# Performance work log

Hardware: AMD Instinct MI355X
Metric: run time of the kernel (lower is better)

The kernel has to match this reference:

```python
import jax, jax.numpy as jnp
import numpy as np

DIM = 64
NUM_HEAD = 4
C_IN = 2 * DIM                      # dim * proj_ratio
N_PER_HEAD = C_IN // NUM_HEAD       # 32
M_TRI = N_PER_HEAD * (N_PER_HEAD + 1) // 2   # 528
C_POOL = NUM_HEAD * M_TRI           # 2112 == dim*(dim+2)/2
EPS = 1e-5


def setup_inputs() -> dict:
    key = jax.random.key(0)
    ks = jax.random.split(key, 8)
    B, H, W = 4, 128, 128
    x = jax.random.normal(ks[0], (B, C_IN, H, W), dtype=jnp.float32)
    norm1_w = 1.0 + 0.1 * jax.random.normal(ks[1], (C_IN,), dtype=jnp.float32)
    norm1_b = 0.1 * jax.random.normal(ks[2], (C_IN,), dtype=jnp.float32)
    dr_w = 0.02 * jax.random.normal(ks[3], (DIM, C_POOL), dtype=jnp.float32)
    dr_b = 0.02 * jax.random.normal(ks[4], (DIM,), dtype=jnp.float32)
    norm2_w = 1.0 + 0.1 * jax.random.normal(ks[5], (DIM,), dtype=jnp.float32)
    norm2_b = 0.1 * jax.random.normal(ks[6], (DIM,), dtype=jnp.float32)
    fc1_w = 0.05 * jax.random.normal(ks[7], (DIM, DIM), dtype=jnp.float32)
    fc1_b = jnp.zeros((DIM,), dtype=jnp.float32)
    return {"x": x, "norm1_w": norm1_w, "norm1_b": norm1_b,
            "dr_w": dr_w, "dr_b": dr_b,
            "norm2_w": norm2_w, "norm2_b": norm2_b,
            "fc1_w": fc1_w, "fc1_b": fc1_b}


def _layernorm_nchw(x, g, b):
    # LayerNorm over channel dim of NCHW tensor (torch permutes to NHWC first)
    xt = jnp.transpose(x, (0, 2, 3, 1))
    mu = jnp.mean(xt, axis=-1, keepdims=True)
    var = jnp.mean(jnp.square(xt - mu), axis=-1, keepdims=True)
    y = (xt - mu) / jnp.sqrt(var + EPS) * g + b
    return jnp.transpose(y, (0, 3, 1, 2))


def reference(x, norm1_w, norm1_b, dr_w, dr_b, norm2_w, norm2_b, fc1_w, fc1_b):
    B, C, H, W = x.shape
    L = H * W
    nh, n = NUM_HEAD, N_PER_HEAD

    # --- norm1 ---
    x = _layernorm_nchw(x, norm1_w, norm1_b)

    # --- MHSP ---
    # channel shuffle: group = C // num_head = n, group_C = num_head
    x = x.reshape(B, n, nh, H, W).transpose(0, 2, 1, 3, 4).reshape(B, C, H, W)
    # unfold with kernel=1, stride=1, pad=0 is a pure reshape -> [B, L, C]
    t = x.reshape(B, C, L).transpose(0, 2, 1).reshape(B, L, nh, n)
    # per-position per-head rank-1 outer product: [B, L, nh, n, n]
    outer = jnp.einsum('blhi,blhj->blhij', t, t)
    # sparse_mapping matmul == gather of upper-triangle entries (row-major i<=j)
    iu, ju = np.triu_indices(n)
    pf = outer[..., iu, ju]                      # [B, L, nh, m]
    pf = pf.reshape(B, L, nh * M_TRI).transpose(0, 2, 1).reshape(B, C_POOL, H, W)

    # --- CTM token mixer ---
    C2 = C_POOL
    y = pf.reshape(B, nh, C2 // nh, L)
    yn = y / jnp.linalg.norm(y, axis=2, keepdims=True)
    mid = L // 2
    x0 = yn[..., mid]                            # [B, nh, C2/nh]
    attn = jnp.einsum('bhc,bhcl->bhl', x0, yn)   # [B, nh, L]
    attn = jax.nn.softmax(attn, axis=-1)[:, :, None, :]
    y = (y * attn * float(L)).reshape(B, C2, H, W)

    # --- dimension reduction (1x1 conv) ---
    z = jnp.einsum('bchw,oc->bohw', y, dr_w) + dr_b[None, :, None, None]

    # --- norm2 + LightMlp (1x1 conv + GELU) ---
    z = _layernorm_nchw(z, norm2_w, norm2_b)
    z = jnp.einsum('bchw,oc->bohw', z, fc1_w) + fc1_b[None, :, None, None]
    z = jax.nn.gelu(z, approximate=False)
    return z
```

## Files before the change

kernel.cpp:

```cpp
#include <hip/hip_runtime.h>
#include <hip/hip_bf16.h>
#include <math.h>

#define B_    4
#define CIN   128
#define L_    16384
#define NH    4
#define NN    32
#define MT    528
#define CP    2112
#define DIM_  64
#define LT    64
#define MID   8192
#define EPS_  1e-5f

#define KPH   640
#define KTOT  2560
#define WSWN  (KTOT * DIM_)
#define FSWN  (2 * 4 * 64 * 8)
#define LOGITS_BLOCKS 1024
#define PREP_BLOCKS   656

typedef __attribute__((ext_vector_type(8))) short short8;
typedef __attribute__((ext_vector_type(4))) float float4v;

__device__ inline unsigned short f2bf(float f) {
  unsigned u = __float_as_uint(f);
  unsigned r = (u + 0x7fffu + ((u >> 16) & 1u)) >> 16;
  return (unsigned short)r;
}
__device__ inline float bf2f(unsigned short h) {
  return __uint_as_float(((unsigned)h) << 16);
}

__device__ inline void kb_decode(int id, int& i, int& jb) {
  if (id < 32)      { i = id >> 2;               jb = id & 3; }
  else if (id < 56) { int r = id - 32; int d = r / 3; i = 8 + d;  jb = 1 + (r - 3 * d); }
  else if (id < 72) { int r = id - 56; i = 16 + (r >> 1); jb = 2 + (r & 1); }
  else              { i = 24 + (id - 72);         jb = 3; }
}

__global__ __launch_bounds__(256) void k_pre(const float* __restrict__ dr_w,
                                             const float* __restrict__ fc1_w,
                                             const float* __restrict__ x,
                                             const float* __restrict__ g1,
                                             const float* __restrict__ b1,
                                             unsigned short* __restrict__ wsw,
                                             unsigned short* __restrict__ fsw,
                                             float* __restrict__ ws_a,
                                             float* __restrict__ ws_bsum) {
  if (blockIdx.x >= LOGITS_BLOCKS) {
    int s = (blockIdx.x - LOGITS_BLOCKS) * 256 + threadIdx.x;
    if (s < WSWN) {
      int j    = s & 7;
      int lane = (s >> 3) & 63;
      int ot   = (s >> 9) & 3;
      int ksg  = s >> 11;
      int o  = ot * 16 + (lane & 15);
      int kp = ksg * 32 + (lane >> 4) * 8 + j;
      int h  = kp / KPH;
      int kk = kp - h * KPH;
      int kb = kk >> 3, jo = kk & 7;
      int i, jb; kb_decode(kb, i, jb);
      int jch = jb * 8 + jo;
      float val = 0.f;
      if (jch >= i) {
        int fi = 32 * i - (i * (i - 1)) / 2;
        int m  = h * MT + fi + (jch - i);
        val = dr_w[(size_t)o * CP + m];
      }
      wsw[s] = f2bf(val);
    } else {
      int s2 = s - WSWN;
      int j    = s2 & 7;
      int lane = (s2 >> 3) & 63;
      int ot   = (s2 >> 9) & 3;
      int ks2  = s2 >> 11;
      int o = ot * 16 + (lane & 15);
      int c = ks2 * 32 + (lane >> 4) * 8 + j;
      fsw[s2] = f2bf(fc1_w[o * DIM_ + c]);
    }
    return;
  }
  int blk = blockIdx.x;
  int b = blk >> 8;
  int l0 = (blk & 255) << 6;
  int t = threadIdx.x;
  int l = t & 63, q = t >> 6;
  __shared__ float xs[CIN], smid[CIN];
  __shared__ float part[4][64], part2[4][64], mu_s[64], isd_s[64];
  __shared__ float musd[2];

  if (t < CIN) xs[t] = x[(size_t)b * CIN * L_ + (size_t)t * L_ + MID];

  float tv[32];
  const float* xb = x + (size_t)b * CIN * L_ + l0 + l;
  float s = 0.f, s2 = 0.f;
#pragma unroll
  for (int cc = 0; cc < 32; cc++) {
    float v = xb[(size_t)(cc * 4 + q) * L_];
    tv[cc] = v; s += v; s2 += v * v;
  }
  part[q][l] = s; part2[q][l] = s2;
  __syncthreads();
  if (t == 0) {
    float su = 0.f;
    for (int c = 0; c < CIN; c++) su += xs[c];
    float mu = su / CIN;
    float sv = 0.f;
    for (int c = 0; c < CIN; c++) { float d = xs[c] - mu; sv += d * d; }
    musd[0] = mu; musd[1] = rsqrtf(sv / CIN + EPS_);
  }
  if (t < 64) {
    float su = part[0][t] + part[1][t] + part[2][t] + part[3][t];
    float su2 = part2[0][t] + part2[1][t] + part2[2][t] + part2[3][t];
    float mu = su * (1.f / CIN);
    float var = su2 * (1.f / CIN) - mu * mu;
    mu_s[t] = mu; isd_s[t] = rsqrtf(var + EPS_);
  }
  __syncthreads();
  if (t < CIN) {
    int c = ((t & 31) << 2) + (t >> 5);
    smid[t] = (xs[c] - musd[0]) * musd[1] * g1[c] + b1[c];
  }
  {
    float mu = mu_s[l], isd = isd_s[l];
#pragma unroll
    for (int cc = 0; cc < 32; cc++) {
      int co = cc * 4 + q;
      tv[cc] = (tv[cc] - mu) * isd * g1[co] + b1[co];
    }
  }
  __syncthreads();
  float T2 = 0.f, T4 = 0.f, st = 0.f, sc2 = 0.f, S2 = 0.f, S4 = 0.f;
#pragma unroll
  for (int i = 0; i < 32; i++) {
    float si = smid[q * 32 + i];
    float ti = tv[i];
    float t2 = ti * ti;
    T2 += t2; T4 = fmaf(t2, t2, T4);
    float ci = si * ti;
    st += ci; sc2 = fmaf(ci, ci, sc2);
    float s2i = si * si;
    S2 += s2i; S4 = fmaf(s2i, s2i, S4);
  }
  float num = 0.5f * (st * st + sc2);
  float logit = num * rsqrtf(0.25f * (T2 * T2 + T4) * (S2 * S2 + S4));
  float e = expf(logit - 1.f);
  ws_a[((size_t)b * NH + q) * L_ + l0 + l] = e;
  float ws = e;
#pragma unroll
  for (int mk = 1; mk < 64; mk <<= 1) ws += __shfl_xor(ws, mk, 64);
  if (l == 0) ws_bsum[((size_t)b * NH + q) * 256 + (blk & 255)] = ws;
}

struct __align__(16) SmemM {
  union __align__(16) { unsigned short p2[4 * 5 * 4 * 16 * 8]; float zb[64 * 65]; } u1;
  union __align__(16) { unsigned short ut[64 * 128]; unsigned short zn2[4 * 2 * 4 * 16 * 8]; } u2;
  float part[4][64], part2[4][64], mu_s[64], isd_s[64];
};

__device__ inline int utidx(int l, int c) {
  return l * 128 + ((((c >> 3) ^ (l & 7))) << 3) + (c & 7);
}

__global__ __launch_bounds__(256, 3) void k_main(const float* __restrict__ x,
      const float* __restrict__ g1, const float* __restrict__ b1,
      const float* __restrict__ dr_b,
      const float* __restrict__ g2, const float* __restrict__ b2,
      const float* __restrict__ fc1_b,
      const unsigned short* __restrict__ wsw, const unsigned short* __restrict__ fsw,
      const float* __restrict__ ws_a, const float* __restrict__ ws_bsum,
      float* __restrict__ out) {
  __shared__ SmemM sm;
  int blk = blockIdx.x;
  int b = blk >> 8;
  int l0 = (blk & 255) << 6;
  int t = threadIdx.x;
  int l = t & 63, q = t >> 6;

  float asum;
  {
    const float* bs = ws_bsum + ((size_t)b * NH + q) * 256;
    float a0 = bs[l] + bs[l + 64] + bs[l + 128] + bs[l + 192];
#pragma unroll
    for (int mk = 1; mk < 64; mk <<= 1) a0 += __shfl_xor(a0, mk, 64);
    asum = a0;
  }
  float e = ws_a[((size_t)b * NH + q) * L_ + l0 + l];
  float sa = sqrtf(e * ((float)L_ / asum));

  const float* xb = x + (size_t)b * CIN * L_ + l0;
  float s = 0.f, s2 = 0.f;
#pragma unroll
  for (int cb = 0; cb < 4; cb++) {
    unsigned short pk[8];
#pragma unroll
    for (int e8 = 0; e8 < 8; e8++) {
      int cc = cb * 8 + e8;
      int co = cc * 4 + q;
      float v = xb[(size_t)co * L_ + l];
      s += v; s2 += v * v;
      pk[e8] = f2bf(v);
    }
    *(short8*)&sm.u2.ut[l * 128 + (((q * 4 + cb) ^ (l & 7)) << 3)] = *(short8*)pk;
  }
  sm.part[q][l] = s; sm.part2[q][l] = s2;
  __syncthreads();
  if (t < 64) {
    float su = sm.part[0][t] + sm.part[1][t] + sm.part[2][t] + sm.part[3][t];
    float su2 = sm.part2[0][t] + sm.part2[1][t] + sm.part2[2][t] + sm.part2[3][t];
    float mu = su * (1.f / CIN);
    float var = su2 * (1.f / CIN) - mu * mu;
    sm.mu_s[t] = mu; sm.isd_s[t] = rsqrtf(var + EPS_);
  }
  __syncthreads();
  {
    float mu = sm.mu_s[l], isd = sm.isd_s[l];
#pragma unroll
    for (int cb = 0; cb < 4; cb++) {
      unsigned short* pp = &sm.u2.ut[l * 128 + (((q * 4 + cb) ^ (l & 7)) << 3)];
      short8 v8 = *(short8*)pp;
      unsigned short pk[8];
#pragma unroll
      for (int e8 = 0; e8 < 8; e8++) {
        int cc = cb * 8 + e8;
        int co = cc * 4 + q;
        float tvv = (bf2f((unsigned short)v8[e8]) - mu) * isd * g1[co] + b1[co];
        pk[e8] = f2bf(tvv * sa);
      }
      *(short8*)pp = *(short8*)pk;
    }
  }
  __syncthreads();

  const int otp = q & 1, ltp = q >> 1;
  const int lta = ltp * 2, ltb = ltp * 2 + 1;
  float4v acc[2][2];
  acc[0][0] = (float4v)0.f; acc[0][1] = (float4v)0.f;
  acc[1][0] = (float4v)0.f; acc[1][1] = (float4v)0.f;
  int tl = l;
  int ltile = l >> 4, n = l & 15;

  for (int cc16 = 0; cc16 < 16; cc16++) {
    int h = cc16 >> 2;
    int cpart = cc16 & 3;
#pragma unroll
    for (int s5 = 0; s5 < 5; s5++) {
      int kbl = q * 5 + s5;
      int kbh = cpart * 20 + kbl;
      int i, jb; kb_decode(kbh, i, jb);
      float ui = bf2f(sm.u2.ut[utidx(l, h * 32 + i)]);
      short8 ub = *(short8*)&sm.u2.ut[l * 128 + (((h * 4 + jb) ^ (l & 7)) << 3)];
      unsigned short pk[8];
#pragma unroll
      for (int e8 = 0; e8 < 8; e8++) pk[e8] = f2bf(ui * bf2f((unsigned short)ub[e8]));
      int ks = kbl >> 2, quad = kbl & 3;
      *(short8*)&sm.u1.p2[(((ltile * 5 + ks) * 4 + quad) * 16 + n) * 8] = *(short8*)pk;
    }
    __syncthreads();
#pragma unroll
    for (int ks = 0; ks < 5; ks++) {
      const unsigned short* wk = wsw + (size_t)(cc16 * 5 + ks) * 2048 + otp * 1024 + tl * 8;
      short8 a0 = *(const short8*)(wk);
      short8 a1 = *(const short8*)(wk + 512);
      short8 b0 = *(short8*)&sm.u1.p2[((lta * 5 + ks) * 64 + tl) * 8];
      short8 b1v = *(short8*)&sm.u1.p2[((ltb * 5 + ks) * 64 + tl) * 8];
      acc[0][0] = __builtin_amdgcn_mfma_f32_16x16x32_bf16(a0, b0,  acc[0][0], 0, 0, 0);
      acc[0][1] = __builtin_amdgcn_mfma_f32_16x16x32_bf16(a0, b1v, acc[0][1], 0, 0, 0);
      acc[1][0] = __builtin_amdgcn_mfma_f32_16x16x32_bf16(a1, b0,  acc[1][0], 0, 0, 0);
      acc[1][1] = __builtin_amdgcn_mfma_f32_16x16x32_bf16(a1, b1v, acc[1][1], 0, 0, 0);
    }
    __syncthreads();
  }

  int quad = tl >> 4;
#pragma unroll
  for (int oi = 0; oi < 2; oi++) {
#pragma unroll
    for (int li = 0; li < 2; li++) {
      int ot = otp * 2 + oi, ltx = ltp * 2 + li;
#pragma unroll
      for (int r = 0; r < 4; r++) {
        int o = ot * 16 + quad * 4 + r;
        sm.u1.zb[(ltx * 16 + n) * 65 + o] = acc[oi][li][r] + dr_b[o];
      }
    }
  }
  __syncthreads();
  {
    float ss = 0.f, ss2 = 0.f;
#pragma unroll
    for (int k = 0; k < 16; k++) {
      float v = sm.u1.zb[l * 65 + q * 16 + k];
      ss += v; ss2 += v * v;
    }
    sm.part[q][l] = ss; sm.part2[q][l] = ss2;
  }
  __syncthreads();
  if (t < 64) {
    float su = sm.part[0][t] + sm.part[1][t] + sm.part[2][t] + sm.part[3][t];
    float su2 = sm.part2[0][t] + sm.part2[1][t] + sm.part2[2][t] + sm.part2[3][t];
    float mu = su * (1.f / DIM_);
    float var = su2 * (1.f / DIM_) - mu * mu;
    sm.mu_s[t] = mu; sm.isd_s[t] = rsqrtf(var + EPS_);
  }
  __syncthreads();
  {
    float mu2 = sm.mu_s[l], isd2 = sm.isd_s[l];
#pragma unroll
    for (int kk = 0; kk < 2; kk++) {
      int kb2 = q * 2 + kk;
      int c0 = kb2 * 8;
      unsigned short pk[8];
#pragma unroll
      for (int e8 = 0; e8 < 8; e8++) {
        int c = c0 + e8;
        float v = (sm.u1.zb[l * 65 + c] - mu2) * isd2 * g2[c] + b2[c];
        pk[e8] = f2bf(v);
      }
      int ks2 = kb2 >> 2, qd2 = kb2 & 3;
      *(short8*)&sm.u2.zn2[(((ltile * 2 + ks2) * 4 + qd2) * 16 + n) * 8] = *(short8*)pk;
    }
  }
  __syncthreads();
  float4v acc2[4];
  acc2[0] = (float4v)0.f; acc2[1] = (float4v)0.f; acc2[2] = (float4v)0.f; acc2[3] = (float4v)0.f;
#pragma unroll
  for (int ks2 = 0; ks2 < 2; ks2++) {
    short8 bz = *(short8*)&sm.u2.zn2[((q * 2 + ks2) * 64 + tl) * 8];
    const unsigned short* fk = fsw + ks2 * 2048 + tl * 8;
    short8 f0 = *(const short8*)(fk);
    short8 f1 = *(const short8*)(fk + 512);
    short8 f2 = *(const short8*)(fk + 1024);
    short8 f3 = *(const short8*)(fk + 1536);
    acc2[0] = __builtin_amdgcn_mfma_f32_16x16x32_bf16(f0, bz, acc2[0], 0, 0, 0);
    acc2[1] = __builtin_amdgcn_mfma_f32_16x16x32_bf16(f1, bz, acc2[1], 0, 0, 0);
    acc2[2] = __builtin_amdgcn_mfma_f32_16x16x32_bf16(f2, bz, acc2[2], 0, 0, 0);
    acc2[3] = __builtin_amdgcn_mfma_f32_16x16x32_bf16(f3, bz, acc2[3], 0, 0, 0);
  }
#pragma unroll
  for (int ot = 0; ot < 4; ot++) {
#pragma unroll
    for (int r = 0; r < 4; r++) {
      int o2 = ot * 16 + quad * 4 + r;
      float sv = acc2[ot][r] + fc1_b[o2];
      float g = 0.5f * sv * (1.f + erff(sv * 0.70710678118f));
      out[((size_t)b * DIM_ + o2) * L_ + l0 + q * 16 + n] = g;
    }
  }
}

extern "C" void kernel_launch(void* const* d_in, const int* in_sizes, int n_in,
                              void* d_out, int out_size, void* d_ws, size_t ws_size,
                              hipStream_t stream) {
  const float* x    = (const float*)d_in[0];
  const float* n1w  = (const float*)d_in[1];
  const float* n1b  = (const float*)d_in[2];
  const float* drw  = (const float*)d_in[3];
  const float* drb  = (const float*)d_in[4];
  const float* n2w  = (const float*)d_in[5];
  const float* n2b  = (const float*)d_in[6];
  const float* fc1w = (const float*)d_in[7];
  const float* fc1b = (const float*)d_in[8];
  float* out = (float*)d_out;
  float* ws = (float*)d_ws;
  float* ws_a    = ws;
  float* ws_bsum = ws_a + (size_t)B_ * NH * L_;
  unsigned short* wsw = (unsigned short*)(ws_bsum + B_ * NH * 256);
  unsigned short* fsw = wsw + WSWN;

  hipLaunchKernelGGL(k_pre, dim3(LOGITS_BLOCKS + PREP_BLOCKS), dim3(256), 0, stream,
                     drw, fc1w, x, n1w, n1b, wsw, fsw, ws_a, ws_bsum);
  hipLaunchKernelGGL(k_main, dim3(B_ * (L_ / LT)), dim3(256), 0, stream,
                     x, n1w, n1b, drb, n2w, n2b, fc1b, wsw, fsw, ws_a, ws_bsum, out);
}
```

Before: 152.2 us.

## Repartition MFMA tiles per wave, pack bf16 pairs with perm, widen LDS swizzle

Each wave now computes all 64 output channels for its own 16-position tile, loading four weight fragments and one LDS B fragment per k-step instead of two of each. This cuts LDS reads of the product tile but doubles global weight loads per wave. Float-to-bf16 conversion now packs two values at once with a single perm on rounded-up bits (round-half-up rather than round-to-nearest-even). The LDS swizzle XOR widens from 8 to 16 lanes, and launch bounds rise to 4 blocks per SIMD, which may raise register pressure or cause spills.

```diff
diff --git a/kernel.cpp b/kernel.cpp
--- a/kernel.cpp
+++ b/kernel.cpp
@@ -31,6 +31,10 @@
 }
 __device__ inline float bf2f(unsigned short h) {
   return __uint_as_float(((unsigned)h) << 16);
+}
+__device__ inline unsigned pack2bf(float a, float b) {
+  return __builtin_amdgcn_perm(__float_as_uint(b) + 0x8000u,
+                               __float_as_uint(a) + 0x8000u, 0x07060302u);
 }
 
 __device__ inline void kb_decode(int id, int& i, int& jb) {
@@ -161,10 +165,10 @@
 };
 
 __device__ inline int utidx(int l, int c) {
-  return l * 128 + ((((c >> 3) ^ (l & 7))) << 3) + (c & 7);
-}
-
-__global__ __launch_bounds__(256, 3) void k_main(const float* __restrict__ x,
+  return l * 128 + ((((c >> 3) ^ (l & 15))) << 3) + (c & 7);
+}
+
+__global__ __launch_bounds__(256, 4) void k_main(const float* __restrict__ x,
       const float* __restrict__ g1, const float* __restrict__ b1,
       const float* __restrict__ dr_b,
       const float* __restrict__ g2, const float* __restrict__ b2,
@@ -194,16 +198,16 @@
   float s = 0.f, s2 = 0.f;
 #pragma unroll
   for (int cb = 0; cb < 4; cb++) {
-    unsigned short pk[8];
-#pragma unroll
-    for (int e8 = 0; e8 < 8; e8++) {
-      int cc = cb * 8 + e8;
-      int co = cc * 4 + q;
-      float v = xb[(size_t)co * L_ + l];
-      s += v; s2 += v * v;
-      pk[e8] = f2bf(v);
-    }
-    *(short8*)&sm.u2.ut[l * 128 + (((q * 4 + cb) ^ (l & 7)) << 3)] = *(short8*)pk;
+    unsigned pk[4];
+#pragma unroll
+    for (int e2 = 0; e2 < 4; e2++) {
+      int cc0 = cb * 8 + 2 * e2;
+      float v0 = xb[(size_t)(cc0 * 4 + q) * L_ + l];
+      float v1 = xb[(size_t)((cc0 + 1) * 4 + q) * L_ + l];
+      s += v0 + v1; s2 += v0 * v0 + v1 * v1;
+      pk[e2] = pack2bf(v0, v1);
+    }
+    *(short8*)&sm.u2.ut[l * 128 + (((q * 4 + cb) ^ (l & 15)) << 3)] = *(short8*)pk;
   }
   sm.part[q][l] = s; sm.part2[q][l] = s2;
   __syncthreads();
@@ -219,26 +223,24 @@
     float mu = sm.mu_s[l], isd = sm.isd_s[l];
 #pragma unroll
     for (int cb = 0; cb < 4; cb++) {
-      unsigned short* pp = &sm.u2.ut[l * 128 + (((q * 4 + cb) ^ (l & 7)) << 3)];
+      unsigned short* pp = &sm.u2.ut[l * 128 + (((q * 4 + cb) ^ (l & 15)) << 3)];
       short8 v8 = *(short8*)pp;
-      unsigned short pk[8];
-#pragma unroll
-      for (int e8 = 0; e8 < 8; e8++) {
-        int cc = cb * 8 + e8;
-        int co = cc * 4 + q;
-        float tvv = (bf2f((unsigned short)v8[e8]) - mu) * isd * g1[co] + b1[co];
-        pk[e8] = f2bf(tvv * sa);
+      unsigned pk[4];
+#pragma unroll
+      for (int e2 = 0; e2 < 4; e2++) {
+        int cc0 = cb * 8 + 2 * e2;
+        int co0 = cc0 * 4 + q, co1 = (cc0 + 1) * 4 + q;
+        float t0 = ((bf2f((unsigned short)v8[2 * e2])     - mu) * isd * g1[co0] + b1[co0]) * sa;
+        float t1 = ((bf2f((unsigned short)v8[2 * e2 + 1]) - mu) * isd * g1[co1] + b1[co1]) * sa;
+        pk[e2] = pack2bf(t0, t1);
       }
       *(short8*)pp = *(short8*)pk;
     }
   }
   __syncthreads();
 
-  const int otp = q & 1, ltp = q >> 1;
-  const int lta = ltp * 2, ltb = ltp * 2 + 1;
-  float4v acc[2][2];
-  acc[0][0] = (float4v)0.f; acc[0][1] = (float4v)0.f;
-  acc[1][0] = (float4v)0.f; acc[1][1] = (float4v)0.f;
+  float4v acc[4];
+  acc[0] = (float4v)0.f; acc[1] = (float4v)0.f; acc[2] = (float4v)0.f; acc[3] = (float4v)0.f;
   int tl = l;
   int ltile = l >> 4, n = l & 15;
 
@@ -251,40 +253,42 @@
       int kbh = cpart * 20 + kbl;
       int i, jb; kb_decode(kbh, i, jb);
       float ui = bf2f(sm.u2.ut[utidx(l, h * 32 + i)]);
-      short8 ub = *(short8*)&sm.u2.ut[l * 128 + (((h * 4 + jb) ^ (l & 7)) << 3)];
-      unsigned short pk[8];
-#pragma unroll
-      for (int e8 = 0; e8 < 8; e8++) pk[e8] = f2bf(ui * bf2f((unsigned short)ub[e8]));
+      short8 ub = *(short8*)&sm.u2.ut[l * 128 + (((h * 4 + jb) ^ (l & 15)) << 3)];
+      unsigned pk[4];
+#pragma unroll
+      for (int e2 = 0; e2 < 4; e2++) {
+        float p0 = ui * bf2f((unsigned short)ub[2 * e2]);
+        float p1 = ui * bf2f((unsigned short)ub[2 * e2 + 1]);
+        pk[e2] = pack2bf(p0, p1);
+      }
       int ks = kbl >> 2, quad = kbl & 3;
       *(short8*)&sm.u1.p2[(((ltile * 5 + ks) * 4 + quad) * 16 + n) * 8] = *(short8*)pk;
     }
     __syncthreads();
+    const unsigned short* wbase = wsw + (size_t)(cc16 * 5) * 2048 + tl * 8;
 #pragma unroll
     for (int ks = 0; ks < 5; ks++) {
-      const unsigned short* wk = wsw + (size_t)(cc16 * 5 + ks) * 2048 + otp * 1024 + tl * 8;
+      short8 bf = *(short8*)&sm.u1.p2[((q * 5 + ks) * 64 + tl) * 8];
+      const unsigned short* wk = wbase + ks * 2048;
       short8 a0 = *(const short8*)(wk);
       short8 a1 = *(const short8*)(wk + 512);
-      short8 b0 = *(short8*)&sm.u1.p2[((lta * 5 + ks) * 64 + tl) * 8];
-      short8 b1v = *(short8*)&sm.u1.p2[((ltb * 5 + ks) * 64 + tl) * 8];
-      acc[0][0] = __builtin_amdgcn_mfma_f32_16x16x32_bf16(a0, b0,  acc[0][0], 0, 0, 0);
-      acc[0][1] = __builtin_amdgcn_mfma_f32_16x16x32_bf16(a0, b1v, acc[0][1], 0, 0, 0);
-      acc[1][0] = __builtin_amdgcn_mfma_f32_16x16x32_bf16(a1, b0,  acc[1][0], 0, 0, 0);
-      acc[1][1] = __builtin_amdgcn_mfma_f32_16x16x32_bf16(a1, b1v, acc[1][1], 0, 0, 0);
+      short8 a2 = *(const short8*)(wk + 1024);
+      short8 a3 = *(const short8*)(wk + 1536);
+      acc[0] = __builtin_amdgcn_mfma_f32_16x16x32_bf16(a0, bf, acc[0], 0, 0, 0);
+      acc[1] = __builtin_amdgcn_mfma_f32_16x16x32_bf16(a1, bf, acc[1], 0, 0, 0);
+      acc[2] = __builtin_amdgcn_mfma_f32_16x16x32_bf16(a2, bf, acc[2], 0, 0, 0);
+      acc[3] = __builtin_amdgcn_mfma_f32_16x16x32_bf16(a3, bf, acc[3], 0, 0, 0);
     }
     __syncthreads();
   }
 
   int quad = tl >> 4;
 #pragma unroll
-  for (int oi = 0; oi < 2; oi++) {
-#pragma unroll
-    for (int li = 0; li < 2; li++) {
-      int ot = otp * 2 + oi, ltx = ltp * 2 + li;
-#pragma unroll
-      for (int r = 0; r < 4; r++) {
-        int o = ot * 16 + quad * 4 + r;
-        sm.u1.zb[(ltx * 16 + n) * 65 + o] = acc[oi][li][r] + dr_b[o];
-      }
+  for (int ot = 0; ot < 4; ot++) {
+#pragma unroll
+    for (int r = 0; r < 4; r++) {
+      int o = ot * 16 + quad * 4 + r;
+      sm.u1.zb[(q * 16 + n) * 65 + o] = acc[ot][r] + dr_b[o];
     }
   }
   __syncthreads();
@@ -312,12 +316,13 @@
     for (int kk = 0; kk < 2; kk++) {
       int kb2 = q * 2 + kk;
       int c0 = kb2 * 8;
-      unsigned short pk[8];
-#pragma unroll
-      for (int e8 = 0; e8 < 8; e8++) {
-        int c = c0 + e8;
-        float v = (sm.u1.zb[l * 65 + c] - mu2) * isd2 * g2[c] + b2[c];
-        pk[e8] = f2bf(v);
+      unsigned pk[4];
+#pragma unroll
+      for (int e2 = 0; e2 < 4; e2++) {
+        int ca = c0 + 2 * e2, cb2 = ca + 1;
+        float va = (sm.u1.zb[l * 65 + ca] - mu2) * isd2 * g2[ca] + b2[ca];
+        float vb = (sm.u1.zb[l * 65 + cb2] - mu2) * isd2 * g2[cb2] + b2[cb2];
+        pk[e2] = pack2bf(va, vb);
       }
       int ks2 = kb2 >> 2, qd2 = kb2 & 3;
       *(short8*)&sm.u2.zn2[(((ltile * 2 + ks2) * 4 + qd2) * 16 + n) * 8] = *(short8*)pk;
```

Result: slower. 157.3 us (+3.4%).
